# Kernel optimization log

Measured on AMD Instinct MI355X. Metric: run time of the kernel, lower is better.

Reference implementation:

```python
import jax, jax.numpy as jnp
import numpy as np

SAMPLE_RATE = 44100
FRAME_SEC = 1.0
NUM_CELLS = 64
SAMPLES_IN_FRAME = int(FRAME_SEC * SAMPLE_RATE)
B, F, N = 128, 512, 64


def setup_inputs() -> dict:
    key = jax.random.key(0)
    k1, k2 = jax.random.split(key)
    # one offset per frame: frame f starts at f*SAMPLES_IN_FRAME, tiled over batch
    offsets = jnp.tile((jnp.arange(F, dtype=jnp.float32) * SAMPLES_IN_FRAME)[None, :], (B, 1))
    starts = offsets[..., None] + jax.random.uniform(k1, (B, F, N), dtype=jnp.float32) * (0.9 * SAMPLES_IN_FRAME)
    durs = jax.random.uniform(k2, (B, F, N), dtype=jnp.float32) * (0.1 * SAMPLES_IN_FRAME)
    frags = jnp.stack([starts, starts + durs], axis=-1)  # [B,F,N,2], end >= start
    return {"frames_of_fragments_batch": frags, "frame_offsets_samples_batch": offsets}


def _resolve_one(fr, sc, ec):
    # fr: [T,2] fragments, sc/ec: [T] int32 grid cells. T static.
    T = fr.shape[0]
    order = jnp.argsort(fr[:, 0])
    fr = fr[order]
    sc = sc[order]
    ec = ec[order]
    # rank 0 if fragment touches grid boundary, else 1
    rank = jnp.where((sc == 0) | (ec == NUM_CELLS - 1), 0, 1).astype(jnp.int32)
    # sorted by start: next fragment intersects current group iff start <= running max end
    cmax = jax.lax.cummax(fr[:, 1], axis=0)
    new_group = jnp.concatenate([jnp.zeros(1, jnp.int32), (fr[1:, 0] > cmax[:-1]).astype(jnp.int32)])
    gid = jnp.cumsum(new_group)  # [T], group ids 0..G-1
    gmax = jax.ops.segment_max(rank, gid, num_segments=T)
    ismax = (rank == gmax[gid]).astype(fr.dtype)
    num = jax.ops.segment_sum(fr * ismax[:, None], gid, num_segments=T)
    cnt = jax.ops.segment_sum(ismax, gid, num_segments=T)
    resolved = num / jnp.maximum(cnt, 1.0)[:, None]  # padded [T,2]; rows >= G are zeros
    return resolved, gid[-1] + 1


def reference(frames_of_fragments_batch, frame_offsets_samples_batch):
    frags = frames_of_fragments_batch  # [B,F,N,2]
    off = frame_offsets_samples_batch[..., None]  # [B,F,1]
    coef = jnp.asarray(NUM_CELLS / SAMPLES_IN_FRAME, dtype=frags.dtype)
    sc = jnp.maximum(0, jnp.floor((frags[..., 0] - off) * coef).astype(jnp.int32))
    ec = jnp.minimum(NUM_CELLS - 1, jnp.floor((frags[..., 1] - off) * coef).astype(jnp.int32))
    Bd, Fd, Nd = frags.shape[:3]
    T = Fd * Nd
    flat = frags.reshape(Bd, T, 2)
    sc = sc.reshape(Bd, T)
    ec = ec.reshape(Bd, T)
    resolved, num_groups = jax.vmap(_resolve_one)(flat, sc, ec)
    return resolved, num_groups
```

## Files before the change

### kernel.cpp

```cpp
#include <hip/hip_runtime.h>

#define NB 128
#define NF 512
#define NFRAG 64
#define NFRAMES (NB * NF)
#define TROWS (NF * NFRAG)

typedef unsigned long long u64;
typedef unsigned int u32;


template<int CTRL, int ROWM, bool BC>
__device__ __forceinline__ int dppi(int x, int old) {
    return __builtin_amdgcn_update_dpp(old, x, CTRL, ROWM, 0xF, BC);
}
template<int CTRL, int ROWM, bool BC>
__device__ __forceinline__ float dppf(float x, float old) {
    return __int_as_float(dppi<CTRL, ROWM, BC>(__float_as_int(x), __float_as_int(old)));
}
template<int OFS>
__device__ __forceinline__ int swzi(int x) {
    return __builtin_amdgcn_ds_swizzle(x, OFS);
}

__device__ __forceinline__ u32 khi(u64 k) { return (u32)(k >> 32); }
__device__ __forceinline__ u32 klo(u64 k) { return (u32)k; }
__device__ __forceinline__ u64 mkk(u32 h, u32 l) { return ((u64)h << 32) | l; }


#define QN 4

#define CMPX_Q(K, J) { \
    bool dsc = ((lane & (K)) != 0) != ((lane & (J)) != 0); \
    _Pragma("unroll") for (int q = 0; q < QN; ++q) { \
        bool sw = dsc != (k2[q] < k[q]); \
        k[q] = sw ? k2[q] : k[q]; } }

#define ST_DPP_Q(K, J, CTRL) { u64 k2[QN]; \
    _Pragma("unroll") for (int q = 0; q < QN; ++q) { \
        u32 h = (u32)dppi<CTRL, 0xF, true>((int)khi(k[q]), (int)khi(k[q])); \
        u32 l = (u32)dppi<CTRL, 0xF, true>((int)klo(k[q]), (int)klo(k[q])); \
        k2[q] = mkk(h, l); } \
    CMPX_Q(K, J) }

#define ST_SWZ_Q(K, J, OFS) { u64 k2[QN]; \
    _Pragma("unroll") for (int q = 0; q < QN; ++q) { \
        u32 h = (u32)swzi<OFS>((int)khi(k[q])); \
        u32 l = (u32)swzi<OFS>((int)klo(k[q])); \
        k2[q] = mkk(h, l); } \
    CMPX_Q(K, J) }

#define ST_SHF_Q(K, J) { u64 k2[QN]; \
    _Pragma("unroll") for (int q = 0; q < QN; ++q) { \
        u32 h = (u32)__shfl_xor((int)khi(k[q]), J, 64); \
        u32 l = (u32)__shfl_xor((int)klo(k[q]), J, 64); \
        k2[q] = mkk(h, l); } \
    CMPX_Q(K, J) }

__device__ __forceinline__ void sort64(u64 (&k)[QN], int lane) {
    ST_DPP_Q(2, 1, 0xB1)
    ST_DPP_Q(4, 2, 0x4E)  ST_DPP_Q(4, 1, 0xB1)
    ST_SWZ_Q(8, 4, 0x101F) ST_DPP_Q(8, 2, 0x4E) ST_DPP_Q(8, 1, 0xB1)
    ST_DPP_Q(16, 8, 0x128) ST_SWZ_Q(16, 4, 0x101F) ST_DPP_Q(16, 2, 0x4E) ST_DPP_Q(16, 1, 0xB1)
    ST_SWZ_Q(32, 16, 0x401F) ST_DPP_Q(32, 8, 0x128) ST_SWZ_Q(32, 4, 0x101F) ST_DPP_Q(32, 2, 0x4E) ST_DPP_Q(32, 1, 0xB1)
    ST_SHF_Q(64, 32)
    ST_SWZ_Q(64, 16, 0x401F) ST_DPP_Q(64, 8, 0x128) ST_SWZ_Q(64, 4, 0x101F) ST_DPP_Q(64, 2, 0x4E) ST_DPP_Q(64, 1, 0xB1)
}


__device__ __forceinline__ void scan_max_q(float (&x)[QN]) {
#define SMSTEP(CTRL, RM, BC) { _Pragma("unroll") for (int q = 0; q < QN; ++q) \
        x[q] = fmaxf(x[q], dppf<CTRL, RM, BC>(x[q], 0.0f)); }
    SMSTEP(0x111, 0xF, true) SMSTEP(0x112, 0xF, true) SMSTEP(0x114, 0xF, true)
    SMSTEP(0x118, 0xF, true) SMSTEP(0x142, 0xA, false) SMSTEP(0x143, 0xC, false)
#undef SMSTEP
}

__device__ __forceinline__ void scan_sum2_q(float (&a)[QN], float (&b)[QN]) {
#define SSSTEP(CTRL, RM, BC) { \
    _Pragma("unroll") for (int q = 0; q < QN; ++q) a[q] += dppf<CTRL, RM, BC>(a[q], 0.0f); \
    _Pragma("unroll") for (int q = 0; q < QN; ++q) b[q] += dppf<CTRL, RM, BC>(b[q], 0.0f); }
    SSSTEP(0x111, 0xF, true) SSSTEP(0x112, 0xF, true) SSSTEP(0x114, 0xF, true)
    SSSTEP(0x118, 0xF, true) SSSTEP(0x142, 0xA, false) SSSTEP(0x143, 0xC, false)
#undef SSSTEP
}

template<int MODE>
__global__ __launch_bounds__(256) void frag_kernel(const float2* __restrict__ frags,
                                                   const float* __restrict__ offsets,
                                                   int* __restrict__ counts,
                                                   const int* __restrict__ offs,
                                                   float2* __restrict__ rows,
                                                   float* __restrict__ out) {
    int lane = threadIdx.x & 63;
    int f0 = (blockIdx.x * 4 + (threadIdx.x >> 6)) * QN;

    const float2* fp = frags + (size_t)f0 * NFRAG + lane;
    u64 k[QN];
#pragma unroll
    for (int q = 0; q < QN; ++q) {
        float2 v = fp[q * NFRAG];
        k[q] = mkk(__float_as_uint(v.x), __float_as_uint(v.y));
    }
    sort64(k, lane);

    float s[QN], e[QN];
#pragma unroll
    for (int q = 0; q < QN; ++q) {
        s[q] = __uint_as_float(khi(k[q]));
        e[q] = __uint_as_float(klo(k[q]));
    }

    float run[QN];
#pragma unroll
    for (int q = 0; q < QN; ++q) run[q] = e[q];
    scan_max_q(run);

    u64 gs[QN];
#pragma unroll
    for (int q = 0; q < QN; ++q) {
        float prev = __shfl_up(run[q], 1, 64);
        bool ng = (s[q] > prev);
        gs[q] = __ballot(ng) | 1ull;
    }

    if (MODE == 2) {
        if (lane == 0) {
            int4 c;
            c.x = (int)__popcll(gs[0]); c.y = (int)__popcll(gs[1]);
            c.z = (int)__popcll(gs[2]); c.w = (int)__popcll(gs[3]);
            *(int4*)(counts + f0) = c;
        }
        return;
    }

    u64 le_mask = ((1ull << lane) << 1) - 1ull;

    float4 offv = *(const float4*)(offsets + f0);
    float offa[QN] = {offv.x, offv.y, offv.z, offv.w};

    bool rank[QN]; u64 r1[QN];
    const float coef = (float)(64.0 / 44100.0);
#pragma unroll
    for (int q = 0; q < QN; ++q) {
        float off = offa[q];
        int sc = (int)floorf((s[q] - off) * coef); if (sc < 0) sc = 0;
        int ec = (int)floorf((e[q] - off) * coef); if (ec > 63) ec = 63;
        rank[q] = (sc != 0 && ec != 63);
        r1[q] = __ballot(rank[q]);
    }

    int startL[QN], endL[QN]; u64 span[QN];
#pragma unroll
    for (int q = 0; q < QN; ++q) {
        startL[q] = 63 - __builtin_clzll(gs[q] & le_mask);
        u64 above = gs[q] & ~le_mask;
        endL[q] = above ? (__builtin_ctzll(above) - 1) : 63;
        span[q] = (((1ull << endL[q]) << 1) - 1ull) & ~((1ull << startL[q]) - 1ull);
    }

    bool ismax[QN]; float cnt[QN];
#pragma unroll
    for (int q = 0; q < QN; ++q) {
        bool gmax = (r1[q] & span[q]) != 0ull;
        ismax[q] = (rank[q] == gmax);
        u64 im = __ballot(ismax[q]);
        cnt[q] = (float)__popcll(im & span[q]);
    }

    float ps[QN], pe[QN];
#pragma unroll
    for (int q = 0; q < QN; ++q) {
        ps[q] = ismax[q] ? s[q] : 0.0f;
        pe[q] = ismax[q] ? e[q] : 0.0f;
    }
    scan_sum2_q(ps, pe);

#pragma unroll
    for (int q = 0; q < QN; ++q) {
        float bs = __shfl(ps[q] - (ismax[q] ? s[q] : 0.0f), startL[q], 64);
        float be = __shfl(pe[q] - (ismax[q] ? e[q] : 0.0f), startL[q], 64);
        int gid = (int)__popcll(gs[q] & le_mask) - 1;
        if (lane == endL[q]) {
            float inv = __builtin_amdgcn_rcpf(cnt[q]);
            float2 r;
            r.x = (ps[q] - bs) * inv;
            r.y = (pe[q] - be) * inv;
            int frame = f0 + q;
            if (MODE == 0) {
                rows[(size_t)frame * NFRAG + gid] = r;
            } else {
                int b = frame >> 9;
                ((float2*)out)[(size_t)b * TROWS + offs[frame] + gid] = r;
            }
        }
    }
    if (MODE == 0 && lane == 0) {
        int4 c;
        c.x = (int)__popcll(gs[0]); c.y = (int)__popcll(gs[1]);
        c.z = (int)__popcll(gs[2]); c.w = (int)__popcll(gs[3]);
        *(int4*)(counts + f0) = c;
    }
}


__global__ __launch_bounds__(64) void scan_kernel(const int* __restrict__ cnt,
                                                  int* __restrict__ offs,
                                                  int* __restrict__ totals,
                                                  float* __restrict__ out_tail) {
    int b = blockIdx.x, lane = threadIdx.x;
    const int4* p = (const int4*)(cnt + b * NF);
    int4 v0 = p[lane * 2], v1 = p[lane * 2 + 1];
    int l[8] = {v0.x, v0.y, v0.z, v0.w, v1.x, v1.y, v1.z, v1.w};
    int pre[8], sum = 0;
#pragma unroll
    for (int kk = 0; kk < 8; ++kk) { pre[kk] = sum; sum += l[kk]; }
    int inc = sum;
    inc += dppi<0x111, 0xF, true>(inc, 0);
    inc += dppi<0x112, 0xF, true>(inc, 0);
    inc += dppi<0x114, 0xF, true>(inc, 0);
    inc += dppi<0x118, 0xF, true>(inc, 0);
    inc += dppi<0x142, 0xA, false>(inc, 0);
    inc += dppi<0x143, 0xC, false>(inc, 0);
    int base = inc - sum;
    int4 o0 = make_int4(base + pre[0], base + pre[1], base + pre[2], base + pre[3]);
    int4 o1 = make_int4(base + pre[4], base + pre[5], base + pre[6], base + pre[7]);
    int4* op = (int4*)(offs + b * NF);
    op[lane * 2] = o0; op[lane * 2 + 1] = o1;
    int total = __builtin_amdgcn_readlane(inc, 63);
    if (lane == 0) { totals[b] = total; out_tail[b] = (float)total; }
}


#define ZBLOCKS (NB * TROWS / 4 / 256)
#define CBLOCKS (NFRAMES / 16)

__global__ __launch_bounds__(256) void finish_kernel(const float2* __restrict__ rows,
                                                     const int* __restrict__ cnt,
                                                     const int* __restrict__ offs,
                                                     const int* __restrict__ totals,
                                                     float* __restrict__ out) {
    if (blockIdx.x < ZBLOCKS) {
        int idx = blockIdx.x * 256 + threadIdx.x;
        int b = idx >> 13;
        int r0 = (idx & 8191) * 4;
        int ng = totals[b];
        float* p = out + ((size_t)b * TROWS + r0) * 2;
        if (r0 >= ng) {
            *(float4*)p = make_float4(0.f, 0.f, 0.f, 0.f);
            *(float4*)(p + 4) = make_float4(0.f, 0.f, 0.f, 0.f);
        } else if (r0 + 4 > ng) {
#pragma unroll
            for (int kk = 1; kk < 4; ++kk)
                if (r0 + kk >= ng) *(float2*)(p + kk * 2) = make_float2(0.f, 0.f);
        }
    } else {
        int lane = threadIdx.x & 63;
        int f0 = ((blockIdx.x - ZBLOCKS) * 4 + (threadIdx.x >> 6)) * QN;
#pragma unroll
        for (int q = 0; q < QN; ++q) {
            int frame = f0 + q;
            int G = cnt[frame];
            if (lane < G) {
                int b = frame >> 9;
                ((float2*)out)[(size_t)b * TROWS + offs[frame] + lane] =
                    rows[(size_t)frame * NFRAG + lane];
            }
        }
    }
}

extern "C" void kernel_launch(void* const* d_in, const int* in_sizes, int n_in,
                              void* d_out, int out_size, void* d_ws, size_t ws_size,
                              hipStream_t stream) {
    const float2* frags = (const float2*)d_in[0];
    const float* offsets = (const float*)d_in[1];
    float* out = (float*)d_out;

    int* counts = (int*)d_ws;
    int* offs = counts + NFRAMES;
    int* totals = offs + NFRAMES;
    float2* rows = (float2*)((char*)d_ws + ((size_t)2 * NFRAMES + NB + 2) * sizeof(int));
    size_t small = ((size_t)2 * NFRAMES + NB + 2) * sizeof(int);
    size_t need = small + (size_t)NFRAMES * NFRAG * sizeof(float2);

    float* tail = out + (size_t)NB * TROWS * 2;

    if (ws_size >= need) {
        frag_kernel<0><<<NFRAMES / 16, 256, 0, stream>>>(frags, offsets, counts, nullptr, rows, nullptr);
        scan_kernel<<<NB, 64, 0, stream>>>(counts, offs, totals, tail);
        finish_kernel<<<ZBLOCKS + CBLOCKS, 256, 0, stream>>>(rows, counts, offs, totals, out);
    } else {
        frag_kernel<2><<<NFRAMES / 16, 256, 0, stream>>>(frags, offsets, counts, nullptr, nullptr, nullptr);
        scan_kernel<<<NB, 64, 0, stream>>>(counts, offs, totals, tail);
        finish_kernel<<<ZBLOCKS, 256, 0, stream>>>(nullptr, nullptr, nullptr, totals, out);
        frag_kernel<1><<<NFRAMES / 16, 256, 0, stream>>>(frags, offsets, counts, offs, nullptr, out);
    }
}
```

Measured before the change: 44.21 us.

## Fuse per-batch scan into finish kernel and simplify rank computation

Removes the separate scan kernel on the workspace path. Each finish block recomputes the batch's 512-frame exclusive prefix sum in shared memory and then does zero-fill or compaction. This saves one kernel launch and the dependency round trip, at the cost of 64 redundant scans per batch. It also replaces the floor/clamp of the cell index with direct float comparisons for the rank test, and caches the masked start/end values so they are not recomputed.

```diff
diff --git a/kernel.cpp b/kernel.cpp
--- a/kernel.cpp
+++ b/kernel.cpp
@@ -143,10 +143,9 @@
     const float coef = (float)(64.0 / 44100.0);
 #pragma unroll
     for (int q = 0; q < QN; ++q) {
-        float off = offa[q];
-        int sc = (int)floorf((s[q] - off) * coef); if (sc < 0) sc = 0;
-        int ec = (int)floorf((e[q] - off) * coef); if (ec > 63) ec = 63;
-        rank[q] = (sc != 0 && ec != 63);
+        float xs_ = (s[q] - offa[q]) * coef;
+        float xe_ = (e[q] - offa[q]) * coef;
+        rank[q] = (xs_ >= 1.0f) && (xe_ < 63.0f);
         r1[q] = __ballot(rank[q]);
     }
 
@@ -168,18 +167,19 @@
         cnt[q] = (float)__popcll(im & span[q]);
     }
 
-    float ps[QN], pe[QN];
-#pragma unroll
-    for (int q = 0; q < QN; ++q) {
-        ps[q] = ismax[q] ? s[q] : 0.0f;
-        pe[q] = ismax[q] ? e[q] : 0.0f;
+    float xs[QN], xe[QN], ps[QN], pe[QN];
+#pragma unroll
+    for (int q = 0; q < QN; ++q) {
+        xs[q] = ismax[q] ? s[q] : 0.0f;
+        xe[q] = ismax[q] ? e[q] : 0.0f;
+        ps[q] = xs[q]; pe[q] = xe[q];
     }
     scan_sum2_q(ps, pe);
 
 #pragma unroll
     for (int q = 0; q < QN; ++q) {
-        float bs = __shfl(ps[q] - (ismax[q] ? s[q] : 0.0f), startL[q], 64);
-        float be = __shfl(pe[q] - (ismax[q] ? e[q] : 0.0f), startL[q], 64);
+        float bs = __shfl(ps[q] - xs[q], startL[q], 64);
+        float be = __shfl(pe[q] - xe[q], startL[q], 64);
         int gid = (int)__popcll(gs[q] & le_mask) - 1;
         if (lane == endL[q]) {
             float inv = __builtin_amdgcn_rcpf(cnt[q]);
@@ -204,13 +204,70 @@
 }
 
 
+template<bool COMPACT>
+__global__ __launch_bounds__(256) void finish_kernel(const float2* __restrict__ rows,
+                                                     const int* __restrict__ cnt,
+                                                     float* __restrict__ out,
+                                                     float* __restrict__ out_tail) {
+    __shared__ int loff[NF + 1];
+    __shared__ int wtot[4];
+    int t = threadIdx.x;
+    int lanel = t & 63, wv = t >> 6;
+    int b = blockIdx.x >> 6, r = blockIdx.x & 63;
+
+    int2 c01 = *(const int2*)(cnt + b * NF + t * 2);
+    int sum2 = c01.x + c01.y;
+    int inc = sum2;
+    inc += dppi<0x111, 0xF, true>(inc, 0);
+    inc += dppi<0x112, 0xF, true>(inc, 0);
+    inc += dppi<0x114, 0xF, true>(inc, 0);
+    inc += dppi<0x118, 0xF, true>(inc, 0);
+    inc += dppi<0x142, 0xA, false>(inc, 0);
+    inc += dppi<0x143, 0xC, false>(inc, 0);
+    if (lanel == 63) wtot[wv] = inc;
+    __syncthreads();
+    int w0 = wtot[0], w1 = wtot[1], w2 = wtot[2], w3 = wtot[3];
+    int base = (wv > 0 ? w0 : 0) + (wv > 1 ? w1 : 0) + (wv > 2 ? w2 : 0);
+    int total = w0 + w1 + w2 + w3;
+    int off0 = base + inc - sum2;
+    loff[t * 2] = off0;
+    loff[t * 2 + 1] = off0 + c01.x;
+    if (t == 255) loff[NF] = total;
+    __syncthreads();
+
+    if (r < 32) {
+        int r0 = (r * 256 + t) * 4;
+        float* p = out + ((size_t)b * TROWS + r0) * 2;
+        if (r0 >= total) {
+            *(float4*)p = make_float4(0.f, 0.f, 0.f, 0.f);
+            *(float4*)(p + 4) = make_float4(0.f, 0.f, 0.f, 0.f);
+        } else if (r0 + 4 > total) {
+#pragma unroll
+            for (int kk = 1; kk < 4; ++kk)
+                if (r0 + kk >= total) *(float2*)(p + kk * 2) = make_float2(0.f, 0.f);
+        }
+        if (r == 0 && t == 0) out_tail[b] = (float)total;
+    } else if (COMPACT) {
+        int fl = (r - 32) * 16 + wv * 4;
+#pragma unroll
+        for (int q = 0; q < 4; ++q) {
+            int fidx = fl + q;
+            int o = loff[fidx];
+            int G = loff[fidx + 1] - o;
+            if (lanel < G) {
+                ((float2*)out)[(size_t)b * TROWS + o + lanel] =
+                    rows[((size_t)b * NF + fidx) * NFRAG + lanel];
+            }
+        }
+    }
+}
+
+
 __global__ __launch_bounds__(64) void scan_kernel(const int* __restrict__ cnt,
-                                                  int* __restrict__ offs,
-                                                  int* __restrict__ totals,
-                                                  float* __restrict__ out_tail) {
-    int b = blockIdx.x, lane = threadIdx.x;
+                                                  int* __restrict__ offs) {
+    int b = blockIdx.x, lanel = threadIdx.x;
     const int4* p = (const int4*)(cnt + b * NF);
-    int4 v0 = p[lane * 2], v1 = p[lane * 2 + 1];
+    int4 v0 = p[lanel * 2], v1 = p[lanel * 2 + 1];
     int l[8] = {v0.x, v0.y, v0.z, v0.w, v1.x, v1.y, v1.z, v1.w};
     int pre[8], sum = 0;
 #pragma unroll
@@ -226,48 +283,7 @@
     int4 o0 = make_int4(base + pre[0], base + pre[1], base + pre[2], base + pre[3]);
     int4 o1 = make_int4(base + pre[4], base + pre[5], base + pre[6], base + pre[7]);
     int4* op = (int4*)(offs + b * NF);
-    op[lane * 2] = o0; op[lane * 2 + 1] = o1;
-    int total = __builtin_amdgcn_readlane(inc, 63);
-    if (lane == 0) { totals[b] = total; out_tail[b] = (float)total; }
-}
-
-
-#define ZBLOCKS (NB * TROWS / 4 / 256)
-#define CBLOCKS (NFRAMES / 16)
-
-__global__ __launch_bounds__(256) void finish_kernel(const float2* __restrict__ rows,
-                                                     const int* __restrict__ cnt,
-                                                     const int* __restrict__ offs,
-                                                     const int* __restrict__ totals,
-                                                     float* __restrict__ out) {
-    if (blockIdx.x < ZBLOCKS) {
-        int idx = blockIdx.x * 256 + threadIdx.x;
-        int b = idx >> 13;
-        int r0 = (idx & 8191) * 4;
-        int ng = totals[b];
-        float* p = out + ((size_t)b * TROWS + r0) * 2;
-        if (r0 >= ng) {
-            *(float4*)p = make_float4(0.f, 0.f, 0.f, 0.f);
-            *(float4*)(p + 4) = make_float4(0.f, 0.f, 0.f, 0.f);
-        } else if (r0 + 4 > ng) {
-#pragma unroll
-            for (int kk = 1; kk < 4; ++kk)
-                if (r0 + kk >= ng) *(float2*)(p + kk * 2) = make_float2(0.f, 0.f);
-        }
-    } else {
-        int lane = threadIdx.x & 63;
-        int f0 = ((blockIdx.x - ZBLOCKS) * 4 + (threadIdx.x >> 6)) * QN;
-#pragma unroll
-        for (int q = 0; q < QN; ++q) {
-            int frame = f0 + q;
-            int G = cnt[frame];
-            if (lane < G) {
-                int b = frame >> 9;
-                ((float2*)out)[(size_t)b * TROWS + offs[frame] + lane] =
-                    rows[(size_t)frame * NFRAG + lane];
-            }
-        }
-    }
+    op[lanel * 2] = o0; op[lanel * 2 + 1] = o1;
 }
 
 extern "C" void kernel_launch(void* const* d_in, const int* in_sizes, int n_in,
@@ -279,21 +295,19 @@
 
     int* counts = (int*)d_ws;
     int* offs = counts + NFRAMES;
-    int* totals = offs + NFRAMES;
-    float2* rows = (float2*)((char*)d_ws + ((size_t)2 * NFRAMES + NB + 2) * sizeof(int));
-    size_t small = ((size_t)2 * NFRAMES + NB + 2) * sizeof(int);
+    float2* rows = (float2*)((char*)d_ws + (size_t)2 * NFRAMES * sizeof(int));
+    size_t small = (size_t)2 * NFRAMES * sizeof(int);
     size_t need = small + (size_t)NFRAMES * NFRAG * sizeof(float2);
 
     float* tail = out + (size_t)NB * TROWS * 2;
 
     if (ws_size >= need) {
         frag_kernel<0><<<NFRAMES / 16, 256, 0, stream>>>(frags, offsets, counts, nullptr, rows, nullptr);
-        scan_kernel<<<NB, 64, 0, stream>>>(counts, offs, totals, tail);
-        finish_kernel<<<ZBLOCKS + CBLOCKS, 256, 0, stream>>>(rows, counts, offs, totals, out);
+        finish_kernel<true><<<NB * 64, 256, 0, stream>>>(rows, counts, out, tail);
     } else {
         frag_kernel<2><<<NFRAMES / 16, 256, 0, stream>>>(frags, offsets, counts, nullptr, nullptr, nullptr);
-        scan_kernel<<<NB, 64, 0, stream>>>(counts, offs, totals, tail);
-        finish_kernel<<<ZBLOCKS, 256, 0, stream>>>(nullptr, nullptr, nullptr, totals, out);
+        scan_kernel<<<NB, 64, 0, stream>>>(counts, offs);
+        finish_kernel<false><<<NB * 64, 256, 0, stream>>>(nullptr, counts, out, tail);
         frag_kernel<1><<<NFRAMES / 16, 256, 0, stream>>>(frags, offsets, counts, offs, nullptr, out);
     }
 }
```

Measured after the change: 40.39 us. 8.7% less time.
